# Kernel tuning notes

Hardware: AMD Instinct MI355X
Metric: run time of the kernel (lower is better)

## Reference

```python
import jax, jax.numpy as jnp
import numpy as np

N_EMBD = 1024
N_HEAD = 16
HEAD_DIM = N_EMBD // N_HEAD  # 64; scale = sqrt(64) = 8


def setup_inputs() -> dict:
    key = jax.random.key(0)
    k0, k1, k2, k3, k4 = jax.random.split(key, 5)
    B, T = 4, 2048
    x = jax.random.normal(k0, (B, T, N_EMBD), dtype=jnp.float32)
    # torch Linear weights are (out,in); we store (in,out) so y = x @ W + b
    W_attn = jax.random.normal(k1, (N_EMBD, 3 * N_EMBD), dtype=jnp.float32) * 0.02
    b_attn = jax.random.normal(k2, (3 * N_EMBD,), dtype=jnp.float32) * 0.02
    W_proj = jax.random.normal(k3, (N_EMBD, N_EMBD), dtype=jnp.float32) * 0.02
    b_proj = jax.random.normal(k4, (N_EMBD,), dtype=jnp.float32) * 0.02
    return {"x": x, "W_attn": W_attn, "b_attn": b_attn,
            "W_proj": W_proj, "b_proj": b_proj}


def reference(x, W_attn, b_attn, W_proj, b_proj):
    B, T, D = x.shape
    scale = 1.0 / np.float32(np.sqrt(HEAD_DIM))
    qkv = x @ W_attn + b_attn                      # [B,T,3D]
    q, k, v = jnp.split(qkv, 3, axis=-1)           # each [B,T,D]
    att = jnp.einsum('bid,bjd->bij', q, k) * scale # [B,T,T]
    causal = jnp.tril(jnp.ones((T, T), dtype=bool))
    att = jnp.where(causal[None, :, :], att, jnp.float32(-jnp.inf))
    att = jax.nn.softmax(att, axis=-1)
    y = jnp.einsum('bij,bjd->bid', att, v)         # [B,T,D]
    return y @ W_proj + b_proj
```

## Files before the change

kernel.cpp:

```cpp
#include <hip/hip_runtime.h>

typedef __attribute__((ext_vector_type(8))) short short8;
typedef __attribute__((ext_vector_type(4))) float f32x4;
typedef __attribute__((ext_vector_type(4))) unsigned short ushort4v;

struct DB0 { static constexpr int value = 0; };
struct DB1 { static constexpr int value = 1; };

__device__ __forceinline__ unsigned short f2bf(float f) {
  unsigned int u = __float_as_uint(f);
  u += 0x7fffu + ((u >> 16) & 1u);
  return (unsigned short)(u >> 16);
}
__device__ __forceinline__ float bf2f(unsigned short h) {
  return __uint_as_float(((unsigned int)h) << 16);
}

__device__ __forceinline__ void gload16(const unsigned short* g, unsigned short* l) {
  __builtin_amdgcn_global_load_lds(
      (const __attribute__((address_space(1))) unsigned int*)g,
      (__attribute__((address_space(3))) unsigned int*)l,
      16, 0, 0);
}

template <int OFF>
__device__ __forceinline__ short8 dsr(unsigned a) {
  short8 r;
  asm volatile("ds_read_b128 %0, %1 offset:%2" : "=v"(r) : "v"(a), "n"(OFF));
  return r;
}

__device__ __forceinline__ void bar() {
  asm volatile("" ::: "memory");
  __builtin_amdgcn_s_barrier();
  asm volatile("" ::: "memory");
}

__global__ __launch_bounds__(256) void conv_x_kernel(const float* __restrict__ x,
                                                     unsigned short* __restrict__ xb) {
  int i = blockIdx.x * 256 + threadIdx.x;
  f32x4 v = ((const f32x4*)x)[i];
  ushort4v o;
  o[0] = f2bf(v[0]); o[1] = f2bf(v[1]); o[2] = f2bf(v[2]); o[3] = f2bf(v[3]);
  ((ushort4v*)xb)[i] = o;
}

__global__ __launch_bounds__(256) void transpose_w_kernel(const float* __restrict__ W,
                                                          unsigned short* __restrict__ Wt,
                                                          int K, int N) {
  __shared__ float tile[32][33];
  int n0 = blockIdx.x * 32, k0 = blockIdx.y * 32;
  int tx = threadIdx.x, ty = threadIdx.y;
#pragma unroll
  for (int j = 0; j < 32; j += 8)
    tile[ty + j][tx] = W[(size_t)(k0 + ty + j) * N + n0 + tx];
  __syncthreads();
#pragma unroll
  for (int j = 0; j < 32; j += 8)
    Wt[(size_t)(n0 + ty + j) * K + k0 + tx] = f2bf(tile[tx][ty + j]);
}

__global__ __launch_bounds__(256) void softmax_kernel(unsigned short* __restrict__ S) {
  int row = blockIdx.x * 4 + (threadIdx.x >> 6);
  int l = threadIdx.x & 63;
  int rl = row & 2047;
  int rend = ((rl >> 7) + 1) << 7;
  unsigned short* p = S + (size_t)row * 2048;
  float v[32];
  float mx = -3e38f;
#pragma unroll
  for (int i = 0; i < 4; i++) {
    int c0 = (i * 64 + l) * 8;
    if (c0 < rend) {
      short8 raw = *(const short8*)&p[c0];
#pragma unroll
      for (int j = 0; j < 8; j++) {
        v[i * 8 + j] = bf2f((unsigned short)raw[j]);
        mx = fmaxf(mx, v[i * 8 + j]);
      }
    } else {
#pragma unroll
      for (int j = 0; j < 8; j++) v[i * 8 + j] = -3e38f;
    }
  }
#pragma unroll
  for (int off = 1; off < 64; off <<= 1) mx = fmaxf(mx, __shfl_xor(mx, off));
  float s = 0.f;
#pragma unroll
  for (int i = 0; i < 32; i++) { v[i] = exp2f((v[i] - mx) * 1.44269504f); s += v[i]; }
#pragma unroll
  for (int off = 1; off < 64; off <<= 1) s += __shfl_xor(s, off);
  float inv = 1.f / s;
#pragma unroll
  for (int i = 0; i < 4; i++) {
    int c0 = (i * 64 + l) * 8;
    if (c0 < rend) {
      short8 o;
#pragma unroll
      for (int j = 0; j < 8; j++) o[j] = (short)f2bf(v[i * 8 + j] * inv);
      *(short8*)&p[c0] = o;
    }
  }
}

template <int OUTBF>
__global__ __launch_bounds__(256) void gemm128_kernel(
    const unsigned short* __restrict__ A, int lda, long long saz,
    const unsigned short* __restrict__ Bt, int ldb, long long sbz,
    void* __restrict__ Cv, int ldc, long long scz,
    const float* __restrict__ bias, int K, float scale, int causal) {
  __shared__ __align__(16) unsigned short lds[2][16384];

  int bx, by, z;
  if (causal == 3) {
    int i = blockIdx.x;
    by = (int)((sqrtf(8.f * i + 1.f) - 1.f) * 0.5f);
    while ((by + 1) * (by + 2) / 2 <= i) by++;
    while (by * (by + 1) / 2 > i) by--;
    bx = i - by * (by + 1) / 2;
    z = blockIdx.y;
  } else if (causal == 4) {
    int gx = gridDim.x, gy = gridDim.y, gz = gridDim.z;
    int total = gx * gy * gz;
    int id = blockIdx.x + blockIdx.y * gx + blockIdx.z * gx * gy;
    int halfn = total >> 1;
    int half = id >= halfn;
    int r = id - half * halfn;
    bx = r % gx;
    int rest = r / gx;
    int by0 = rest % gy;
    z = rest / gy + half * (gz >> 1);
    by = half ? (gy - 1 - by0) : by0;
  } else {
    bx = blockIdx.x; by = blockIdx.y; z = blockIdx.z;
    int gx = gridDim.x, gy = gridDim.y;
    if (causal == 0 && (gx & 7) == 0 && (gy & 7) == 0) {
      int id = by * gx + bx;
      int s = id >> 6, w = id & 63;
      int spx = gx >> 3;
      bx = (s % spx) * 8 + (w & 7);
      by = (s / spx) * 8 + (w >> 3);
    }
  }
  const int m0 = by * 128, n0 = bx * 128;
  A += (size_t)z * saz;
  Bt += (size_t)z * sbz;

  const int t = threadIdx.x;
  const int lane = t & 63, wid = t >> 6;
  const int g = lane >> 4, q = lane & 15;
  const int wm = wid >> 1, wn = wid & 1;

  int NT = K >> 6;
  if (causal == 1) { if (n0 >= m0 + 128) NT = 0; }
  else if (causal == 2 || causal == 4) { NT = min(K, m0 + 128) >> 6; }

  f32x4 acc[4][4] = {};

  if (NT > 0) {
    const int scol = ((t & 7) * 8) ^ (((t >> 3) & 7) << 3);
    const unsigned short* aS = A + (size_t)(m0 + (t >> 3)) * lda + scol;
    const unsigned short* bS = Bt + (size_t)(n0 + (t >> 3)) * ldb + scol;

    auto stage = [&](int tt) {
      unsigned short* d = &lds[tt & 1][wid * 512];
      const unsigned short* sa = aS + (size_t)tt * 64;
      const unsigned short* sb = bS + (size_t)tt * 64;
      gload16(sa, d);
      gload16(sa + (size_t)32 * lda, d + 2048);
      gload16(sa + (size_t)64 * lda, d + 4096);
      gload16(sa + (size_t)96 * lda, d + 6144);
      gload16(sb, d + 8192);
      gload16(sb + (size_t)32 * ldb, d + 10240);
      gload16(sb + (size_t)64 * ldb, d + 12288);
      gload16(sb + (size_t)96 * ldb, d + 14336);
    };

    const unsigned base =
        (unsigned)(unsigned long long)(__attribute__((address_space(3))) unsigned short*)&lds[0][0];
    const int W = (q & 7) << 4;
    const int colA0 = (g * 16) ^ W;
    const int colA1 = colA0 ^ 64;
    const unsigned aa0B = base + (unsigned)((wm * 64 + q) * 128 + colA0);
    const unsigned aa1B = base + (unsigned)((wm * 64 + q) * 128 + colA1);
    const unsigned bb0B = base + 16384u + (unsigned)((wn * 64 + q) * 128 + colA0);
    const unsigned bb1B = base + 16384u + (unsigned)((wn * 64 + q) * 128 + colA1);

    stage(0);
    if (NT > 1) {
      stage(1);
      asm volatile("s_waitcnt vmcnt(8)" ::: "memory");
    } else {
      asm volatile("s_waitcnt vmcnt(0)" ::: "memory");
    }
    bar();

    auto body = [&](auto dbc, int tt) {
      constexpr int DB = decltype(dbc)::value;
      const unsigned aa0 = aa0B + DB * 32768u, aa1 = aa1B + DB * 32768u;
      const unsigned bb0 = bb0B + DB * 32768u, bb1 = bb1B + DB * 32768u;
      short8 aq[4][2], bq[4][2];
      aq[0][0] = dsr<0>(aa0);    aq[0][1] = dsr<0>(aa1);
      aq[1][0] = dsr<2048>(aa0); aq[1][1] = dsr<2048>(aa1);
      aq[2][0] = dsr<4096>(aa0); aq[2][1] = dsr<4096>(aa1);
      aq[3][0] = dsr<6144>(aa0); aq[3][1] = dsr<6144>(aa1);
      bq[0][0] = dsr<0>(bb0);    bq[0][1] = dsr<0>(bb1);
      bq[1][0] = dsr<2048>(bb0); bq[1][1] = dsr<2048>(bb1);
      bq[2][0] = dsr<4096>(bb0); bq[2][1] = dsr<4096>(bb1);
      bq[3][0] = dsr<6144>(bb0); bq[3][1] = dsr<6144>(bb1);
      asm volatile("s_waitcnt lgkmcnt(0)" ::: "memory");
      __builtin_amdgcn_sched_barrier(0);
      bar();
      if (tt + 2 < NT) stage(tt + 2);
      __builtin_amdgcn_s_setprio(1);
#pragma unroll
      for (int ks = 0; ks < 2; ks++)
#pragma unroll
        for (int m = 0; m < 4; m++)
#pragma unroll
          for (int n = 0; n < 4; n++)
            acc[m][n] = __builtin_amdgcn_mfma_f32_16x16x32_bf16(aq[m][ks], bq[n][ks], acc[m][n], 0, 0, 0);
      __builtin_amdgcn_s_setprio(0);
      __builtin_amdgcn_sched_barrier(0);
      if (tt + 2 < NT) {
        asm volatile("s_waitcnt vmcnt(8)" ::: "memory");
      } else {
        asm volatile("s_waitcnt vmcnt(0)" ::: "memory");
      }
      bar();
    };

    int tt = 0;
    for (; tt + 2 <= NT; tt += 2) {
      body(DB0{}, tt);
      body(DB1{}, tt + 1);
    }
    if (tt < NT) body(DB0{}, tt);
  }

  const bool maskC = (causal == 1) || (causal == 3);
#pragma unroll
  for (int n = 0; n < 4; n++) {
    int colg = n0 + wn * 64 + n * 16 + q;
    float bv = bias ? bias[colg] : 0.f;
#pragma unroll
    for (int m = 0; m < 4; m++) {
      int rowb = m0 + wm * 64 + m * 16 + g * 4;
#pragma unroll
      for (int r = 0; r < 4; r++) {
        float val = acc[m][n][r] * scale + bv;
        if (maskC && colg > rowb + r) val = -1e30f;
        if (OUTBF) {
          ((unsigned short*)Cv)[(size_t)z * scz + (size_t)(rowb + r) * ldc + colg] = f2bf(val);
        } else {
          ((float*)Cv)[(size_t)z * scz + (size_t)(rowb + r) * ldc + colg] = val;
        }
      }
    }
  }
}

extern "C" void kernel_launch(void* const* d_in, const int* in_sizes, int n_in,
                              void* d_out, int out_size, void* d_ws, size_t ws_size,
                              hipStream_t stream) {
  const float* x  = (const float*)d_in[0];
  const float* Wa = (const float*)d_in[1];
  const float* ba = (const float*)d_in[2];
  const float* Wp = (const float*)d_in[3];
  const float* bp = (const float*)d_in[4];
  float* out = (float*)d_out;

  char* ws = (char*)d_ws;
  unsigned short* qkv = (unsigned short*)(ws);
  unsigned short* xb  = (unsigned short*)(ws + 50331648);
  unsigned short* vt  = (unsigned short*)(ws + 50331648);
  unsigned short* wta = (unsigned short*)(ws + 67108864);
  unsigned short* S   = (unsigned short*)(ws + 73400320);
  unsigned short* wtp = (unsigned short*)(ws + 123731968);

  conv_x_kernel<<<8192, 256, 0, stream>>>(x, xb);
  transpose_w_kernel<<<dim3(96, 32), dim3(32, 8), 0, stream>>>(Wa, wta, 1024, 3072);
  transpose_w_kernel<<<dim3(32, 32), dim3(32, 8), 0, stream>>>(Wp, wtp, 1024, 1024);

  gemm128_kernel<1><<<dim3(24, 64, 1), 256, 0, stream>>>(
      xb, 1024, 0, wta, 1024, 0, qkv, 3072, 0, ba, 1024, 1.0f, 0);

  gemm128_kernel<1><<<dim3(136, 4), 256, 0, stream>>>(
      qkv, 3072, 2048LL * 3072, qkv + 1024, 3072, 2048LL * 3072,
      S, 2048, 2048LL * 2048, nullptr, 1024, 0.125f, 3);

  softmax_kernel<<<2048, 256, 0, stream>>>(S);

  gemm128_kernel<1><<<dim3(16, 8, 4), 256, 0, stream>>>(
      wtp, 1024, 0, qkv + 2048, 3072, 2048LL * 3072,
      vt, 2048, 2048LL * 1024, nullptr, 1024, 1.0f, 0);

  gemm128_kernel<0><<<dim3(8, 16, 4), 256, 0, stream>>>(
      S, 2048, 2048LL * 2048, vt, 2048, 2048LL * 1024,
      out, 1024, 2048LL * 1024, bp, 2048, 1.0f, 4);
}
```

Before: 197.8 us.

## Switch GEMM to triple-buffered BK=32 pipeline and merge prep kernels

The GEMM main loop now uses a K-tile of 32 instead of 64 with three LDS buffers. Each tile's global loads are issued one step ahead, and a single barrier per iteration replaces two. LDS use drops from 64KB to 48KB and launch_bounds asks for 3 blocks per CU to raise occupancy. The three input conversion and transpose kernels are merged into one launch, and the 8x8 block-swizzle for L2 locality in the non-causal GEMM is removed, which may cost some cache reuse.

```diff
diff --git a/kernel.cpp b/kernel.cpp
--- a/kernel.cpp
+++ b/kernel.cpp
@@ -6,6 +6,7 @@
 
 struct DB0 { static constexpr int value = 0; };
 struct DB1 { static constexpr int value = 1; };
+struct DB2 { static constexpr int value = 2; };
 
 __device__ __forceinline__ unsigned short f2bf(float f) {
   unsigned int u = __float_as_uint(f);
@@ -36,21 +37,29 @@
   asm volatile("" ::: "memory");
 }
 
-__global__ __launch_bounds__(256) void conv_x_kernel(const float* __restrict__ x,
-                                                     unsigned short* __restrict__ xb) {
-  int i = blockIdx.x * 256 + threadIdx.x;
-  f32x4 v = ((const f32x4*)x)[i];
-  ushort4v o;
-  o[0] = f2bf(v[0]); o[1] = f2bf(v[1]); o[2] = f2bf(v[2]); o[3] = f2bf(v[3]);
-  ((ushort4v*)xb)[i] = o;
-}
-
-__global__ __launch_bounds__(256) void transpose_w_kernel(const float* __restrict__ W,
-                                                          unsigned short* __restrict__ Wt,
-                                                          int K, int N) {
+__global__ __launch_bounds__(256) void prep_kernel(
+    const float* __restrict__ x, unsigned short* __restrict__ xb,
+    const float* __restrict__ Wa, unsigned short* __restrict__ wta,
+    const float* __restrict__ Wp, unsigned short* __restrict__ wtp) {
+  int b = blockIdx.x;
+  int tx = threadIdx.x & 31, ty = threadIdx.x >> 5;
+  if (b < 8192) {
+    int i = b * 256 + threadIdx.x;
+    f32x4 v = ((const f32x4*)x)[i];
+    ushort4v o;
+    o[0] = f2bf(v[0]); o[1] = f2bf(v[1]); o[2] = f2bf(v[2]); o[3] = f2bf(v[3]);
+    ((ushort4v*)xb)[i] = o;
+    return;
+  }
+  const float* W; unsigned short* Wt; int K, N, n0, k0;
+  if (b < 8192 + 3072) {
+    int bb = b - 8192; W = Wa; Wt = wta; K = 1024; N = 3072;
+    n0 = (bb % 96) * 32; k0 = (bb / 96) * 32;
+  } else {
+    int bb = b - 11264; W = Wp; Wt = wtp; K = 1024; N = 1024;
+    n0 = (bb % 32) * 32; k0 = (bb / 32) * 32;
+  }
   __shared__ float tile[32][33];
-  int n0 = blockIdx.x * 32, k0 = blockIdx.y * 32;
-  int tx = threadIdx.x, ty = threadIdx.y;
 #pragma unroll
   for (int j = 0; j < 32; j += 8)
     tile[ty + j][tx] = W[(size_t)(k0 + ty + j) * N + n0 + tx];
@@ -104,12 +113,12 @@
 }
 
 template <int OUTBF>
-__global__ __launch_bounds__(256) void gemm128_kernel(
+__global__ __launch_bounds__(256, 3) void gemm128_kernel(
     const unsigned short* __restrict__ A, int lda, long long saz,
     const unsigned short* __restrict__ Bt, int ldb, long long sbz,
     void* __restrict__ Cv, int ldc, long long scz,
     const float* __restrict__ bias, int K, float scale, int causal) {
-  __shared__ __align__(16) unsigned short lds[2][16384];
+  __shared__ __align__(16) unsigned short lds[3][8192];
 
   int bx, by, z;
   if (causal == 3) {
@@ -133,14 +142,6 @@
     by = half ? (gy - 1 - by0) : by0;
   } else {
     bx = blockIdx.x; by = blockIdx.y; z = blockIdx.z;
-    int gx = gridDim.x, gy = gridDim.y;
-    if (causal == 0 && (gx & 7) == 0 && (gy & 7) == 0) {
-      int id = by * gx + bx;
-      int s = id >> 6, w = id & 63;
-      int spx = gx >> 3;
-      bx = (s % spx) * 8 + (w & 7);
-      by = (s / spx) * 8 + (w >> 3);
-    }
   }
   const int m0 = by * 128, n0 = bx * 128;
   A += (size_t)z * saz;
@@ -151,91 +152,75 @@
   const int g = lane >> 4, q = lane & 15;
   const int wm = wid >> 1, wn = wid & 1;
 
-  int NT = K >> 6;
+  int NT = K >> 5;
   if (causal == 1) { if (n0 >= m0 + 128) NT = 0; }
-  else if (causal == 2 || causal == 4) { NT = min(K, m0 + 128) >> 6; }
+  else if (causal == 2 || causal == 4) { NT = min(K, m0 + 128) >> 5; }
 
   f32x4 acc[4][4] = {};
 
   if (NT > 0) {
-    const int scol = ((t & 7) * 8) ^ (((t >> 3) & 7) << 3);
-    const unsigned short* aS = A + (size_t)(m0 + (t >> 3)) * lda + scol;
-    const unsigned short* bS = Bt + (size_t)(n0 + (t >> 3)) * ldb + scol;
-
-    auto stage = [&](int tt) {
-      unsigned short* d = &lds[tt & 1][wid * 512];
-      const unsigned short* sa = aS + (size_t)tt * 64;
-      const unsigned short* sb = bS + (size_t)tt * 64;
+    const int scol = ((t & 3) ^ ((t >> 3) & 3)) * 8;
+    const unsigned short* aS = A + (size_t)(m0 + (t >> 2)) * lda + scol;
+    const unsigned short* bS = Bt + (size_t)(n0 + (t >> 2)) * ldb + scol;
+
+    auto stage = [&](int tt, int buf) {
+      unsigned short* d = &lds[buf][wid * 512];
+      const unsigned short* sa = aS + (size_t)tt * 32;
+      const unsigned short* sb = bS + (size_t)tt * 32;
       gload16(sa, d);
-      gload16(sa + (size_t)32 * lda, d + 2048);
-      gload16(sa + (size_t)64 * lda, d + 4096);
-      gload16(sa + (size_t)96 * lda, d + 6144);
-      gload16(sb, d + 8192);
-      gload16(sb + (size_t)32 * ldb, d + 10240);
-      gload16(sb + (size_t)64 * ldb, d + 12288);
-      gload16(sb + (size_t)96 * ldb, d + 14336);
+      gload16(sa + (size_t)64 * lda, d + 2048);
+      gload16(sb, d + 4096);
+      gload16(sb + (size_t)64 * ldb, d + 6144);
     };
 
     const unsigned base =
         (unsigned)(unsigned long long)(__attribute__((address_space(3))) unsigned short*)&lds[0][0];
-    const int W = (q & 7) << 4;
-    const int colA0 = (g * 16) ^ W;
-    const int colA1 = colA0 ^ 64;
-    const unsigned aa0B = base + (unsigned)((wm * 64 + q) * 128 + colA0);
-    const unsigned aa1B = base + (unsigned)((wm * 64 + q) * 128 + colA1);
-    const unsigned bb0B = base + 16384u + (unsigned)((wn * 64 + q) * 128 + colA0);
-    const unsigned bb1B = base + 16384u + (unsigned)((wn * 64 + q) * 128 + colA1);
-
-    stage(0);
-    if (NT > 1) {
-      stage(1);
-      asm volatile("s_waitcnt vmcnt(8)" ::: "memory");
-    } else {
-      asm volatile("s_waitcnt vmcnt(0)" ::: "memory");
-    }
-    bar();
+    const int cb = ((g ^ ((q >> 1) & 3)) << 4);
+    const unsigned aaB = base + (unsigned)((wm * 64 + q) * 64 + cb);
+    const unsigned bbB = base + 8192u + (unsigned)((wn * 64 + q) * 64 + cb);
+
+    stage(0, 0);
 
     auto body = [&](auto dbc, int tt) {
       constexpr int DB = decltype(dbc)::value;
-      const unsigned aa0 = aa0B + DB * 32768u, aa1 = aa1B + DB * 32768u;
-      const unsigned bb0 = bb0B + DB * 32768u, bb1 = bb1B + DB * 32768u;
-      short8 aq[4][2], bq[4][2];
-      aq[0][0] = dsr<0>(aa0);    aq[0][1] = dsr<0>(aa1);
-      aq[1][0] = dsr<2048>(aa0); aq[1][1] = dsr<2048>(aa1);
-      aq[2][0] = dsr<4096>(aa0); aq[2][1] = dsr<4096>(aa1);
-      aq[3][0] = dsr<6144>(aa0); aq[3][1] = dsr<6144>(aa1);
-      bq[0][0] = dsr<0>(bb0);    bq[0][1] = dsr<0>(bb1);
-      bq[1][0] = dsr<2048>(bb0); bq[1][1] = dsr<2048>(bb1);
-      bq[2][0] = dsr<4096>(bb0); bq[2][1] = dsr<4096>(bb1);
-      bq[3][0] = dsr<6144>(bb0); bq[3][1] = dsr<6144>(bb1);
-      asm volatile("s_waitcnt lgkmcnt(0)" ::: "memory");
-      __builtin_amdgcn_sched_barrier(0);
-      bar();
-      if (tt + 2 < NT) stage(tt + 2);
-      __builtin_amdgcn_s_setprio(1);
-#pragma unroll
-      for (int ks = 0; ks < 2; ks++)
-#pragma unroll
-        for (int m = 0; m < 4; m++)
-#pragma unroll
-          for (int n = 0; n < 4; n++)
-            acc[m][n] = __builtin_amdgcn_mfma_f32_16x16x32_bf16(aq[m][ks], bq[n][ks], acc[m][n], 0, 0, 0);
-      __builtin_amdgcn_s_setprio(0);
-      __builtin_amdgcn_sched_barrier(0);
-      if (tt + 2 < NT) {
-        asm volatile("s_waitcnt vmcnt(8)" ::: "memory");
+      if (tt + 1 < NT) {
+        stage(tt + 1, (DB + 1) % 3);
+        asm volatile("s_waitcnt vmcnt(4)" ::: "memory");
       } else {
         asm volatile("s_waitcnt vmcnt(0)" ::: "memory");
       }
       bar();
+      const unsigned aa = aaB + DB * 16384u;
+      const unsigned bb = bbB + DB * 16384u;
+      short8 aq[4], bq[4];
+      aq[0] = dsr<0>(aa);
+      aq[1] = dsr<1024>(aa);
+      aq[2] = dsr<2048>(aa);
+      aq[3] = dsr<3072>(aa);
+      bq[0] = dsr<0>(bb);
+      bq[1] = dsr<1024>(bb);
+      bq[2] = dsr<2048>(bb);
+      bq[3] = dsr<3072>(bb);
+      asm volatile("s_waitcnt lgkmcnt(0)" ::: "memory");
+      __builtin_amdgcn_sched_barrier(0);
+      __builtin_amdgcn_s_setprio(1);
+#pragma unroll
+      for (int m = 0; m < 4; m++)
+#pragma unroll
+        for (int n = 0; n < 4; n++)
+          acc[m][n] = __builtin_amdgcn_mfma_f32_16x16x32_bf16(aq[m], bq[n], acc[m][n], 0, 0, 0);
+      __builtin_amdgcn_s_setprio(0);
+      __builtin_amdgcn_sched_barrier(0);
     };
 
     int tt = 0;
-    for (; tt + 2 <= NT; tt += 2) {
+    for (; tt + 3 <= NT; tt += 3) {
       body(DB0{}, tt);
       body(DB1{}, tt + 1);
+      body(DB2{}, tt + 2);
     }
     if (tt < NT) body(DB0{}, tt);
+    if (tt + 1 < NT) body(DB1{}, tt + 1);
   }
 
   const bool maskC = (causal == 1) || (causal == 3);
@@ -278,9 +263,7 @@
   unsigned short* S   = (unsigned short*)(ws + 73400320);
   unsigned short* wtp = (unsigned short*)(ws + 123731968);
 
-  conv_x_kernel<<<8192, 256, 0, stream>>>(x, xb);
-  transpose_w_kernel<<<dim3(96, 32), dim3(32, 8), 0, stream>>>(Wa, wta, 1024, 3072);
-  transpose_w_kernel<<<dim3(32, 32), dim3(32, 8), 0, stream>>>(Wp, wtp, 1024, 1024);
+  prep_kernel<<<12288, 256, 0, stream>>>(x, xb, Wa, wta, Wp, wtp);
 
   gemm128_kernel<1><<<dim3(24, 64, 1), 256, 0, stream>>>(
       xb, 1024, 0, wta, 1024, 0, qkv, 3072, 0, ba, 1024, 1.0f, 0);
```

Result: no change. 200.5 us (+1.4%).

## Merge prep kernels, simplify GEMM pipeline to one-stage prefetch and drop tile swizzle

Applied to the files above, without the earlier changes.

Folds the x conversion and both weight transposes into one prep launch to cut launch overhead. In the GEMM it removes the grouped tile remap for the non-causal case and switches to a simpler XOR swizzle using a single base address with an immediate offset. It also changes the pipeline from two-tile-ahead prefetch with partial vmcnt waits to one-tile-ahead prefetch with full waits and a single barrier per step. This exposes more global-load latency and may add LDS bank conflicts in exchange for fewer barriers and instructions.

```diff
diff --git a/kernel.cpp b/kernel.cpp
--- a/kernel.cpp
+++ b/kernel.cpp
@@ -36,21 +36,29 @@
   asm volatile("" ::: "memory");
 }
 
-__global__ __launch_bounds__(256) void conv_x_kernel(const float* __restrict__ x,
-                                                     unsigned short* __restrict__ xb) {
-  int i = blockIdx.x * 256 + threadIdx.x;
-  f32x4 v = ((const f32x4*)x)[i];
-  ushort4v o;
-  o[0] = f2bf(v[0]); o[1] = f2bf(v[1]); o[2] = f2bf(v[2]); o[3] = f2bf(v[3]);
-  ((ushort4v*)xb)[i] = o;
-}
-
-__global__ __launch_bounds__(256) void transpose_w_kernel(const float* __restrict__ W,
-                                                          unsigned short* __restrict__ Wt,
-                                                          int K, int N) {
+__global__ __launch_bounds__(256) void prep_kernel(
+    const float* __restrict__ x, unsigned short* __restrict__ xb,
+    const float* __restrict__ Wa, unsigned short* __restrict__ wta,
+    const float* __restrict__ Wp, unsigned short* __restrict__ wtp) {
+  int b = blockIdx.x;
+  int tx = threadIdx.x & 31, ty = threadIdx.x >> 5;
+  if (b < 8192) {
+    int i = b * 256 + threadIdx.x;
+    f32x4 v = ((const f32x4*)x)[i];
+    ushort4v o;
+    o[0] = f2bf(v[0]); o[1] = f2bf(v[1]); o[2] = f2bf(v[2]); o[3] = f2bf(v[3]);
+    ((ushort4v*)xb)[i] = o;
+    return;
+  }
+  const float* W; unsigned short* Wt; int K, N, n0, k0;
+  if (b < 8192 + 3072) {
+    int bb = b - 8192; W = Wa; Wt = wta; K = 1024; N = 3072;
+    n0 = (bb % 96) * 32; k0 = (bb / 96) * 32;
+  } else {
+    int bb = b - 11264; W = Wp; Wt = wtp; K = 1024; N = 1024;
+    n0 = (bb % 32) * 32; k0 = (bb / 32) * 32;
+  }
   __shared__ float tile[32][33];
-  int n0 = blockIdx.x * 32, k0 = blockIdx.y * 32;
-  int tx = threadIdx.x, ty = threadIdx.y;
 #pragma unroll
   for (int j = 0; j < 32; j += 8)
     tile[ty + j][tx] = W[(size_t)(k0 + ty + j) * N + n0 + tx];
@@ -133,14 +141,6 @@
     by = half ? (gy - 1 - by0) : by0;
   } else {
     bx = blockIdx.x; by = blockIdx.y; z = blockIdx.z;
-    int gx = gridDim.x, gy = gridDim.y;
-    if (causal == 0 && (gx & 7) == 0 && (gy & 7) == 0) {
-      int id = by * gx + bx;
-      int s = id >> 6, w = id & 63;
-      int spx = gx >> 3;
-      bx = (s % spx) * 8 + (w & 7);
-      by = (s / spx) * 8 + (w >> 3);
-    }
   }
   const int m0 = by * 128, n0 = bx * 128;
   A += (size_t)z * saz;
@@ -152,13 +152,12 @@
   const int wm = wid >> 1, wn = wid & 1;
 
   int NT = K >> 6;
-  if (causal == 1) { if (n0 >= m0 + 128) NT = 0; }
-  else if (causal == 2 || causal == 4) { NT = min(K, m0 + 128) >> 6; }
+  if (causal == 4) NT = min(K, m0 + 128) >> 6;
 
   f32x4 acc[4][4] = {};
 
   if (NT > 0) {
-    const int scol = ((t & 7) * 8) ^ (((t >> 3) & 7) << 3);
+    const int scol = ((t & 7) * 8) ^ ((t & 32) >> 1);
     const unsigned short* aS = A + (size_t)(m0 + (t >> 3)) * lda + scol;
     const unsigned short* bS = Bt + (size_t)(n0 + (t >> 3)) * ldb + scol;
 
@@ -178,40 +177,32 @@
 
     const unsigned base =
         (unsigned)(unsigned long long)(__attribute__((address_space(3))) unsigned short*)&lds[0][0];
-    const int W = (q & 7) << 4;
-    const int colA0 = (g * 16) ^ W;
-    const int colA1 = colA0 ^ 64;
-    const unsigned aa0B = base + (unsigned)((wm * 64 + q) * 128 + colA0);
-    const unsigned aa1B = base + (unsigned)((wm * 64 + q) * 128 + colA1);
-    const unsigned bb0B = base + 16384u + (unsigned)((wn * 64 + q) * 128 + colA0);
-    const unsigned bb1B = base + 16384u + (unsigned)((wn * 64 + q) * 128 + colA1);
+    const int colA = (g * 16) ^ ((q & 4) << 3);
+    const unsigned aaB = base + (unsigned)((wm * 64 + q) * 128 + colA);
+    const unsigned bbB = base + 16384u + (unsigned)((wn * 64 + q) * 128 + colA);
 
     stage(0);
-    if (NT > 1) {
-      stage(1);
-      asm volatile("s_waitcnt vmcnt(8)" ::: "memory");
-    } else {
-      asm volatile("s_waitcnt vmcnt(0)" ::: "memory");
-    }
+    asm volatile("s_waitcnt vmcnt(0)" ::: "memory");
     bar();
 
     auto body = [&](auto dbc, int tt) {
       constexpr int DB = decltype(dbc)::value;
-      const unsigned aa0 = aa0B + DB * 32768u, aa1 = aa1B + DB * 32768u;
-      const unsigned bb0 = bb0B + DB * 32768u, bb1 = bb1B + DB * 32768u;
+      const unsigned aa = aaB + DB * 32768u;
+      const unsigned bb = bbB + DB * 32768u;
+      if (tt + 1 < NT) stage(tt + 1);
       short8 aq[4][2], bq[4][2];
-      aq[0][0] = dsr<0>(aa0);    aq[0][1] = dsr<0>(aa1);
-      aq[1][0] = dsr<2048>(aa0); aq[1][1] = dsr<2048>(aa1);
-      aq[2][0] = dsr<4096>(aa0); aq[2][1] = dsr<4096>(aa1);
-      aq[3][0] = dsr<6144>(aa0); aq[3][1] = dsr<6144>(aa1);
-      bq[0][0] = dsr<0>(bb0);    bq[0][1] = dsr<0>(bb1);
-      bq[1][0] = dsr<2048>(bb0); bq[1][1] = dsr<2048>(bb1);
-      bq[2][0] = dsr<4096>(bb0); bq[2][1] = dsr<4096>(bb1);
-      bq[3][0] = dsr<6144>(bb0); bq[3][1] = dsr<6144>(bb1);
+#pragma unroll
+      for (int m = 0; m < 4; m++) {
+        aq[m][0] = dsr<0>(aa + m * 2048u);
+        aq[m][1] = dsr<64>(aa + m * 2048u);
+      }
+#pragma unroll
+      for (int n = 0; n < 4; n++) {
+        bq[n][0] = dsr<0>(bb + n * 2048u);
+        bq[n][1] = dsr<64>(bb + n * 2048u);
+      }
       asm volatile("s_waitcnt lgkmcnt(0)" ::: "memory");
       __builtin_amdgcn_sched_barrier(0);
-      bar();
-      if (tt + 2 < NT) stage(tt + 2);
       __builtin_amdgcn_s_setprio(1);
 #pragma unroll
       for (int ks = 0; ks < 2; ks++)
@@ -222,11 +213,7 @@
             acc[m][n] = __builtin_amdgcn_mfma_f32_16x16x32_bf16(aq[m][ks], bq[n][ks], acc[m][n], 0, 0, 0);
       __builtin_amdgcn_s_setprio(0);
       __builtin_amdgcn_sched_barrier(0);
-      if (tt + 2 < NT) {
-        asm volatile("s_waitcnt vmcnt(8)" ::: "memory");
-      } else {
-        asm volatile("s_waitcnt vmcnt(0)" ::: "memory");
-      }
+      asm volatile("s_waitcnt vmcnt(0)" ::: "memory");
       bar();
     };
 
@@ -238,7 +225,7 @@
     if (tt < NT) body(DB0{}, tt);
   }
 
-  const bool maskC = (causal == 1) || (causal == 3);
+  const bool maskC = (causal == 3);
 #pragma unroll
   for (int n = 0; n < 4; n++) {
     int colg = n0 + wn * 64 + n * 16 + q;
@@ -278,9 +265,7 @@
   unsigned short* S   = (unsigned short*)(ws + 73400320);
   unsigned short* wtp = (unsigned short*)(ws + 123731968);
 
-  conv_x_kernel<<<8192, 256, 0, stream>>>(x, xb);
-  transpose_w_kernel<<<dim3(96, 32), dim3(32, 8), 0, stream>>>(Wa, wta, 1024, 3072);
-  transpose_w_kernel<<<dim3(32, 32), dim3(32, 8), 0, stream>>>(Wp, wtp, 1024, 1024);
+  prep_kernel<<<12288, 256, 0, stream>>>(x, xb, Wa, wta, Wp, wtp);
 
   gemm128_kernel<1><<<dim3(24, 64, 1), 256, 0, stream>>>(
       xb, 1024, 0, wta, 1024, 0, qkv, 3072, 0, ba, 1024, 1.0f, 0);
```

After: 190.9 us. -3.5%, faster.
